# Kernel tuning notes

Hardware: AMD Instinct MI355X
Metric: run time of the kernel (lower is better)

## Reference

```python
import jax, jax.numpy as jnp
import numpy as np

EPS = 1e-8  # torch F.cosine_similarity default eps (norms clamped to >= eps)

def setup_inputs() -> dict:
    key = jax.random.key(0)
    k1, k2 = jax.random.split(key)
    N, K, d = 262144, 512, 128
    X = jax.random.normal(k1, (N, d), dtype=jnp.float32)
    muK = jax.random.normal(k2, (K, d), dtype=jnp.float32)
    return {"X": X, "muK": muK}

def reference(X, muK):
    # Faithful to NCMOpenMax.predict with distance='cosine', return_probas=True:
    # scores[n,k] = cos(X[n], muK[k]); probas = softmax(scores, axis=1).
    # Computed without the N x K x d broadcast intermediate: normalize then matmul.
    xn = X / jnp.maximum(jnp.linalg.norm(X, axis=1, keepdims=True), EPS)
    mn = muK / jnp.maximum(jnp.linalg.norm(muK, axis=1, keepdims=True), EPS)
    scores = jnp.einsum('nd,kd->nk', xn, mn)  # [N, K] cosine similarities
    probas = jax.nn.softmax(scores, axis=1)
    return probas
```

## Files before the change

### kernel.cpp

```cpp
#include <hip/hip_runtime.h>
#include <hip/hip_bf16.h>


using floatx4 = __attribute__((ext_vector_type(4))) float;
using shortx8 = __attribute__((ext_vector_type(8))) short;

__device__ __forceinline__ short f2bf(float f) {
  unsigned u = __builtin_bit_cast(unsigned, f);
  u += 0x7fffu + ((u >> 16) & 1u);
  return (short)(u >> 16);
}

__global__ void norm_mu_kernel(const float* __restrict__ muK, short* __restrict__ mn) {
  int gid  = blockIdx.x * blockDim.x + threadIdx.x;
  int row  = gid >> 6;
  int lane = gid & 63;
  if (row >= 512) return;
  float2 v = ((const float2*)(muK + row * 128))[lane];
  float ss = v.x * v.x + v.y * v.y;
#pragma unroll
  for (int m = 32; m >= 1; m >>= 1) ss += __shfl_xor(ss, m, 64);
  float inv = rsqrtf(fmaxf(ss, 1e-16f));
  short2 o;
  o.x = f2bf(v.x * inv);
  o.y = f2bf(v.y * inv);
  ((short2*)(mn + row * 128))[lane] = o;
}

__global__ __launch_bounds__(256, 2)
void cos_softmax_kernel(const float* __restrict__ X,
                        const short* __restrict__ mn,
                        float* __restrict__ out) {
  const int lane = threadIdx.x & 63;
  const int wave = threadIdx.x >> 6;
  const int c15  = lane & 15;
  const int quad = lane >> 4;
  const int rb   = blockIdx.x * 64;
  const int cb   = wave * 128;

  floatx4 acc[4][8];
#pragma unroll
  for (int rt = 0; rt < 4; ++rt)
#pragma unroll
    for (int ct = 0; ct < 8; ++ct)
      acc[rt][ct] = (floatx4){0.f, 0.f, 0.f, 0.f};

  float sumsq[4] = {0.f, 0.f, 0.f, 0.f};

#pragma unroll
  for (int kk = 0; kk < 4; ++kk) {
    shortx8 afr[4];
#pragma unroll
    for (int rt = 0; rt < 4; ++rt) {
      const float* p = X + (size_t)(rb + rt * 16 + c15) * 128 + kk * 32 + quad * 8;
      float4 u0 = *(const float4*)p;
      float4 u1 = *(const float4*)(p + 4);
      sumsq[rt] += u0.x * u0.x + u0.y * u0.y + u0.z * u0.z + u0.w * u0.w
                 + u1.x * u1.x + u1.y * u1.y + u1.z * u1.z + u1.w * u1.w;
      afr[rt] = (shortx8){ f2bf(u0.x), f2bf(u0.y), f2bf(u0.z), f2bf(u0.w),
                           f2bf(u1.x), f2bf(u1.y), f2bf(u1.z), f2bf(u1.w) };
    }
    shortx8 bfr[8];
#pragma unroll
    for (int ct = 0; ct < 8; ++ct) {
      const short* p = mn + (size_t)(cb + ct * 16 + c15) * 128 + kk * 32 + quad * 8;
      bfr[ct] = *(const shortx8*)p;
    }
#pragma unroll
    for (int rt = 0; rt < 4; ++rt)
#pragma unroll
      for (int ct = 0; ct < 8; ++ct)
        acc[rt][ct] = __builtin_amdgcn_mfma_f32_16x16x32_bf16(afr[rt], bfr[ct], acc[rt][ct], 0, 0, 0);
  }

#pragma unroll
  for (int rt = 0; rt < 4; ++rt) {
    sumsq[rt] += __shfl_xor(sumsq[rt], 16, 64);
    sumsq[rt] += __shfl_xor(sumsq[rt], 32, 64);
  }

  float psum[4][4];
#pragma unroll
  for (int rt = 0; rt < 4; ++rt) {
    float inv[4];
#pragma unroll
    for (int reg = 0; reg < 4; ++reg) {
      float n2 = __shfl(sumsq[rt], (lane & 48) | (quad * 4 + reg), 64);
      inv[reg] = rsqrtf(fmaxf(n2, 1e-16f));
      psum[rt][reg] = 0.f;
    }
#pragma unroll
    for (int ct = 0; ct < 8; ++ct)
#pragma unroll
      for (int reg = 0; reg < 4; ++reg) {
        float e = __expf(acc[rt][ct][reg] * inv[reg]);
        acc[rt][ct][reg] = e;
        psum[rt][reg] += e;
      }
#pragma unroll
    for (int reg = 0; reg < 4; ++reg) {
#pragma unroll
      for (int m = 1; m <= 8; m <<= 1)
        psum[rt][reg] += __shfl_xor(psum[rt][reg], m, 64);
    }
  }

  __shared__ float wsum[4][64];
  __shared__ float tot[64];
  if (c15 == 0) {
#pragma unroll
    for (int rt = 0; rt < 4; ++rt)
#pragma unroll
      for (int reg = 0; reg < 4; ++reg)
        wsum[wave][rt * 16 + quad * 4 + reg] = psum[rt][reg];
  }
  __syncthreads();
  if (threadIdx.x < 64)
    tot[threadIdx.x] = wsum[0][threadIdx.x] + wsum[1][threadIdx.x]
                     + wsum[2][threadIdx.x] + wsum[3][threadIdx.x];
  __syncthreads();

#pragma unroll
  for (int rt = 0; rt < 4; ++rt) {
    float rtot[4];
#pragma unroll
    for (int reg = 0; reg < 4; ++reg)
      rtot[reg] = 1.0f / tot[rt * 16 + quad * 4 + reg];
#pragma unroll
    for (int ct = 0; ct < 8; ++ct) {
      float* po = out + (size_t)(rb + rt * 16 + quad * 4) * 512 + cb + ct * 16 + c15;
#pragma unroll
      for (int reg = 0; reg < 4; ++reg)
        __builtin_nontemporal_store(acc[rt][ct][reg] * rtot[reg], po + (size_t)reg * 512);
    }
  }
}

extern "C" void kernel_launch(void* const* d_in, const int* in_sizes, int n_in,
                              void* d_out, int out_size, void* d_ws, size_t ws_size,
                              hipStream_t stream) {
  const float* X   = (const float*)d_in[0];
  const float* muK = (const float*)d_in[1];
  float* out = (float*)d_out;
  short* mn  = (short*)d_ws;

  norm_mu_kernel<<<128, 256, 0, stream>>>(muK, mn);
  cos_softmax_kernel<<<4096, 256, 0, stream>>>(X, mn, out);
}
```

Before: 837.8 us.

## Transpose MFMA operands so output rows map to lanes for float4 stores

Swaps the A/B operands of the MFMA so the accumulator holds scores transposed: each lane now owns one sample row and four consecutive class columns. This lets the output be written as 16-byte float4 stores instead of scalar nontemporal stores, and it removes the per-register shuffles that broadcast norms and the 16-lane row-sum reductions. The nontemporal hint is dropped, and each float4 store now covers one output row per lane.

```diff
diff --git a/kernel.cpp b/kernel.cpp
--- a/kernel.cpp
+++ b/kernel.cpp
@@ -35,84 +35,75 @@
   const int wave = threadIdx.x >> 6;
   const int c15  = lane & 15;
   const int quad = lane >> 4;
-  const int rb   = blockIdx.x * 64;
-  const int cb   = wave * 128;
+  const int nb   = blockIdx.x * 64;
+  const int kb   = wave * 128;
 
-  floatx4 acc[4][8];
+  floatx4 acc[8][4];
 #pragma unroll
-  for (int rt = 0; rt < 4; ++rt)
+  for (int kt = 0; kt < 8; ++kt)
 #pragma unroll
-    for (int ct = 0; ct < 8; ++ct)
-      acc[rt][ct] = (floatx4){0.f, 0.f, 0.f, 0.f};
+    for (int nt = 0; nt < 4; ++nt)
+      acc[kt][nt] = (floatx4){0.f, 0.f, 0.f, 0.f};
 
   float sumsq[4] = {0.f, 0.f, 0.f, 0.f};
 
 #pragma unroll
   for (int kk = 0; kk < 4; ++kk) {
-    shortx8 afr[4];
+    shortx8 bfr[4];
 #pragma unroll
-    for (int rt = 0; rt < 4; ++rt) {
-      const float* p = X + (size_t)(rb + rt * 16 + c15) * 128 + kk * 32 + quad * 8;
+    for (int nt = 0; nt < 4; ++nt) {
+      const float* p = X + (size_t)(nb + nt * 16 + c15) * 128 + kk * 32 + quad * 8;
       float4 u0 = *(const float4*)p;
       float4 u1 = *(const float4*)(p + 4);
-      sumsq[rt] += u0.x * u0.x + u0.y * u0.y + u0.z * u0.z + u0.w * u0.w
+      sumsq[nt] += u0.x * u0.x + u0.y * u0.y + u0.z * u0.z + u0.w * u0.w
                  + u1.x * u1.x + u1.y * u1.y + u1.z * u1.z + u1.w * u1.w;
-      afr[rt] = (shortx8){ f2bf(u0.x), f2bf(u0.y), f2bf(u0.z), f2bf(u0.w),
+      bfr[nt] = (shortx8){ f2bf(u0.x), f2bf(u0.y), f2bf(u0.z), f2bf(u0.w),
                            f2bf(u1.x), f2bf(u1.y), f2bf(u1.z), f2bf(u1.w) };
     }
-    shortx8 bfr[8];
+    shortx8 afr[8];
 #pragma unroll
-    for (int ct = 0; ct < 8; ++ct) {
-      const short* p = mn + (size_t)(cb + ct * 16 + c15) * 128 + kk * 32 + quad * 8;
-      bfr[ct] = *(const shortx8*)p;
+    for (int kt = 0; kt < 8; ++kt) {
+      const short* p = mn + (size_t)(kb + kt * 16 + c15) * 128 + kk * 32 + quad * 8;
+      afr[kt] = *(const shortx8*)p;
     }
 #pragma unroll
-    for (int rt = 0; rt < 4; ++rt)
+    for (int kt = 0; kt < 8; ++kt)
 #pragma unroll
-      for (int ct = 0; ct < 8; ++ct)
-        acc[rt][ct] = __builtin_amdgcn_mfma_f32_16x16x32_bf16(afr[rt], bfr[ct], acc[rt][ct], 0, 0, 0);
+      for (int nt = 0; nt < 4; ++nt)
+        acc[kt][nt] = __builtin_amdgcn_mfma_f32_16x16x32_bf16(afr[kt], bfr[nt], acc[kt][nt], 0, 0, 0);
   }
 
+  float inv[4];
 #pragma unroll
-  for (int rt = 0; rt < 4; ++rt) {
-    sumsq[rt] += __shfl_xor(sumsq[rt], 16, 64);
-    sumsq[rt] += __shfl_xor(sumsq[rt], 32, 64);
+  for (int nt = 0; nt < 4; ++nt) {
+    sumsq[nt] += __shfl_xor(sumsq[nt], 16, 64);
+    sumsq[nt] += __shfl_xor(sumsq[nt], 32, 64);
+    inv[nt] = rsqrtf(fmaxf(sumsq[nt], 1e-16f));
   }
 
-  float psum[4][4];
+  float psum[4] = {0.f, 0.f, 0.f, 0.f};
 #pragma unroll
-  for (int rt = 0; rt < 4; ++rt) {
-    float inv[4];
+  for (int kt = 0; kt < 8; ++kt)
 #pragma unroll
-    for (int reg = 0; reg < 4; ++reg) {
-      float n2 = __shfl(sumsq[rt], (lane & 48) | (quad * 4 + reg), 64);
-      inv[reg] = rsqrtf(fmaxf(n2, 1e-16f));
-      psum[rt][reg] = 0.f;
-    }
-#pragma unroll
-    for (int ct = 0; ct < 8; ++ct)
+    for (int nt = 0; nt < 4; ++nt)
 #pragma unroll
       for (int reg = 0; reg < 4; ++reg) {
-        float e = __expf(acc[rt][ct][reg] * inv[reg]);
-        acc[rt][ct][reg] = e;
-        psum[rt][reg] += e;
+        float e = __expf(acc[kt][nt][reg] * inv[nt]);
+        acc[kt][nt][reg] = e;
+        psum[nt] += e;
       }
 #pragma unroll
-    for (int reg = 0; reg < 4; ++reg) {
-#pragma unroll
-      for (int m = 1; m <= 8; m <<= 1)
-        psum[rt][reg] += __shfl_xor(psum[rt][reg], m, 64);
-    }
+  for (int nt = 0; nt < 4; ++nt) {
+    psum[nt] += __shfl_xor(psum[nt], 16, 64);
+    psum[nt] += __shfl_xor(psum[nt], 32, 64);
   }
 
   __shared__ float wsum[4][64];
   __shared__ float tot[64];
-  if (c15 == 0) {
+  if (quad == 0) {
 #pragma unroll
-    for (int rt = 0; rt < 4; ++rt)
-#pragma unroll
-      for (int reg = 0; reg < 4; ++reg)
-        wsum[wave][rt * 16 + quad * 4 + reg] = psum[rt][reg];
+    for (int nt = 0; nt < 4; ++nt)
+      wsum[wave][nt * 16 + c15] = psum[nt];
   }
   __syncthreads();
   if (threadIdx.x < 64)
@@ -120,20 +111,22 @@
                      + wsum[2][threadIdx.x] + wsum[3][threadIdx.x];
   __syncthreads();
 
+  float rtot[4];
 #pragma unroll
-  for (int rt = 0; rt < 4; ++rt) {
-    float rtot[4];
+  for (int nt = 0; nt < 4; ++nt)
+    rtot[nt] = 1.0f / tot[nt * 16 + c15];
+
 #pragma unroll
-    for (int reg = 0; reg < 4; ++reg)
-      rtot[reg] = 1.0f / tot[rt * 16 + quad * 4 + reg];
+  for (int kt = 0; kt < 8; ++kt)
 #pragma unroll
-    for (int ct = 0; ct < 8; ++ct) {
-      float* po = out + (size_t)(rb + rt * 16 + quad * 4) * 512 + cb + ct * 16 + c15;
-#pragma unroll
-      for (int reg = 0; reg < 4; ++reg)
-        __builtin_nontemporal_store(acc[rt][ct][reg] * rtot[reg], po + (size_t)reg * 512);
+    for (int nt = 0; nt < 4; ++nt) {
+      float4 o;
+      o.x = acc[kt][nt][0] * rtot[nt];
+      o.y = acc[kt][nt][1] * rtot[nt];
+      o.z = acc[kt][nt][2] * rtot[nt];
+      o.w = acc[kt][nt][3] * rtot[nt];
+      *(float4*)(out + (size_t)(nb + nt * 16 + c15) * 512 + kb + kt * 16 + quad * 4) = o;
     }
-  }
 }
 
 extern "C" void kernel_launch(void* const* d_in, const int* in_sizes, int n_in,
```

Result: slower. 865.5 us (+3.3%).
